# Optimization experiments

Hardware: AMD Instinct MI355X
Metric: run time of the kernel (lower is better)

The kernel has to match this reference:

```python
import jax, jax.numpy as jnp
import numpy as np

EMBED_DIM = 1024
NUM_HEADS = 16
HEAD_DIM = EMBED_DIM // NUM_HEADS
SCALING_FACTOR = 0.1
SCALING = (HEAD_DIM * SCALING_FACTOR) ** (-0.5)
B, L = 4, 1024


def setup_inputs() -> dict:
    key = jax.random.key(0)
    ks = jax.random.split(key, 8)
    query = jax.random.normal(ks[0], (B, L, EMBED_DIM), dtype=jnp.float32)
    key_padding_mask = jnp.zeros((B, L), dtype=bool)
    attn_bias = jax.random.normal(ks[1], (B * NUM_HEADS, L, L), dtype=jnp.float32)
    s_in = 1.0 / np.sqrt(EMBED_DIM)
    Wqkv = jax.random.normal(ks[2], (3 * EMBED_DIM, EMBED_DIM), dtype=jnp.float32) * s_in
    bqkv = jnp.zeros((3 * EMBED_DIM,), dtype=jnp.float32)
    Wo = jax.random.normal(ks[3], (EMBED_DIM, EMBED_DIM), dtype=jnp.float32) * s_in
    bo = jnp.zeros((EMBED_DIM,), dtype=jnp.float32)
    return {"query": query, "key_padding_mask": key_padding_mask, "attn_bias": attn_bias,
            "Wqkv": Wqkv, "bqkv": bqkv, "Wo": Wo, "bo": bo}


def reference(query, key_padding_mask, attn_bias, Wqkv, bqkv, Wo, bo):
    b, l, e = query.shape
    # fused in-projection: (B, L, 3E)
    qkv = jnp.einsum("ble,fe->blf", query, Wqkv) + bqkv
    q, k, v = jnp.split(qkv, 3, axis=-1)
    q = q * SCALING
    # (B, L, H, D)
    q = q.reshape(b, l, NUM_HEADS, HEAD_DIM)
    k = k.reshape(b, l, NUM_HEADS, HEAD_DIM)
    v = v.reshape(b, l, NUM_HEADS, HEAD_DIM)
    # scores: (B, H, L, L)
    scores = jnp.einsum("blhd,bmhd->bhlm", q, k)
    scores = scores + attn_bias.reshape(b, NUM_HEADS, l, l)
    neg_inf = jnp.asarray(-jnp.inf, scores.dtype)
    scores = jnp.where(key_padding_mask[:, None, None, :], neg_inf, scores)
    probs = jax.nn.softmax(scores, axis=-1)  # dropout: eval mode (identity)
    out = jnp.einsum("bhlm,bmhd->blhd", probs, v).reshape(b, l, e)
    return jnp.einsum("ble,fe->blf", out, Wo) + bo
```

## Files before the change

kernel.cpp:

```cpp
#include <hip/hip_runtime.h>
#include <math.h>

#define EMB   1024
#define NH    16
#define HD    64
#define BATCH 4
#define LSEQ  1024
#define NTOK  (BATCH*LSEQ)
#define SCALING 0.39528470752104744f

typedef __attribute__((ext_vector_type(8))) short short8;
typedef __attribute__((ext_vector_type(4))) float f32x4;

__device__ __forceinline__ float bf2f(short s) {
    union { float f; unsigned u; } x; x.u = ((unsigned)(unsigned short)s) << 16; return x.f;
}
__device__ __forceinline__ short f2bf(float f) {
    union { float f; unsigned u; } x; x.f = f;
    unsigned r = x.u + 0x7fff + ((x.u >> 16) & 1);
    return (short)(r >> 16);
}

__device__ __forceinline__ void glds16(const void* g, void* l) {
    __builtin_amdgcn_global_load_lds(
        (const __attribute__((address_space(1))) void*)g,
        (__attribute__((address_space(3))) void*)l, 16, 0, 0);
}

__global__ __launch_bounds__(256) void cvt_bf16(
    const float* __restrict__ in, short* __restrict__ out, int n)
{
    int i = (blockIdx.x * 256 + threadIdx.x) * 8;
    if (i >= n) return;
    float4 a = *(const float4*)(in + i);
    float4 b = *(const float4*)(in + i + 4);
    short8 o;
    o[0] = f2bf(a.x); o[1] = f2bf(a.y); o[2] = f2bf(a.z); o[3] = f2bf(a.w);
    o[4] = f2bf(b.x); o[5] = f2bf(b.y); o[6] = f2bf(b.z); o[7] = f2bf(b.w);
    *(short8*)(out + i) = o;
}

__global__ __launch_bounds__(256) void qkv_gemm(
    const short* __restrict__ X, const short* __restrict__ W,
    const float* __restrict__ bqkv,
    short* __restrict__ qws, short* __restrict__ kws, short* __restrict__ vws)
{
    __shared__ short As[128 * 32];
    __shared__ short Bs[128 * 32];
    const int tid = threadIdx.x;
    const int wave = tid >> 6, lane = tid & 63;
    const int quad = lane >> 4, l16 = lane & 15;
    const int m0 = blockIdx.y * 128, n0 = blockIdx.x * 128;
    const int wm = (wave >> 1) * 64, wn = (wave & 1) * 64;

    f32x4 acc[4][4] = {};

    const int srow = wave * 16 + (lane >> 2);
    const int scol = (lane & 3) * 16;

    const char* gA = (const char*)X + (size_t)(m0 + srow) * 2048 + scol;
    const char* gB = (const char*)W + (size_t)(n0 + srow) * 2048 + scol;
    char* lA = (char*)As + wave * 1024 + lane * 16;
    char* lB = (char*)Bs + wave * 1024 + lane * 16;

    for (int kt = 0; kt < 1024; kt += 32) {
        __syncthreads();
        const char* ga = gA + kt * 2;
        const char* gb = gB + kt * 2;
        glds16(ga, lA);
        glds16(ga + (size_t)64 * 2048, lA + 4096);
        glds16(gb, lB);
        glds16(gb + (size_t)64 * 2048, lB + 4096);
        __syncthreads();

        short8 af[4], bf[4];
        #pragma unroll
        for (int i = 0; i < 4; i++)
            af[i] = *(const short8*)((const char*)As + (wm + i * 16 + l16) * 64 + quad * 16);
        #pragma unroll
        for (int j = 0; j < 4; j++)
            bf[j] = *(const short8*)((const char*)Bs + (wn + j * 16 + l16) * 64 + quad * 16);
        #pragma unroll
        for (int i = 0; i < 4; i++)
            #pragma unroll
            for (int j = 0; j < 4; j++)
                acc[i][j] = __builtin_amdgcn_mfma_f32_16x16x32_bf16(af[i], bf[j], acc[i][j], 0, 0, 0);
    }

    #pragma unroll
    for (int i = 0; i < 4; i++) {
        #pragma unroll
        for (int j = 0; j < 4; j++) {
            #pragma unroll
            for (int r = 0; r < 4; r++) {
                int gm = m0 + wm + i * 16 + quad * 4 + r;
                int gn = n0 + wn + j * 16 + l16;
                float v = acc[i][j][r] + bqkv[gn];
                int part = gn >> 10;
                int cc = gn & 1023;
                int h = cc >> 6, d = cc & 63;
                int b = gm >> 10, l = gm & 1023;
                size_t dst = (((size_t)(b * NH + h)) * LSEQ + l) * HD + d;
                if (part == 0)      qws[dst] = f2bf(v * SCALING);
                else if (part == 1) kws[dst] = f2bf(v);
                else                vws[dst] = f2bf(v);
            }
        }
    }
}

__global__ __launch_bounds__(256) void attn_kernel(
    const short* __restrict__ qws, const short* __restrict__ kws,
    const short* __restrict__ vws, const float* __restrict__ bias,
    const unsigned char* __restrict__ mask, short* __restrict__ att)
{
    __shared__ short Qs[64 * 72];
    __shared__ short Ks[128 * 72];
    __shared__ short Vt[64 * 136];
    __shared__ short Ps[4 * 16 * 136];

    const int qt = blockIdx.x;
    const int bh = blockIdx.y;
    const int b = bh >> 4;
    const int tid = threadIdx.x, wave = tid >> 6, lane = tid & 63;
    const int quad = lane >> 4, l16 = lane & 15;
    const int h = bh & 15;

    const short* Qg = qws + (size_t)bh * LSEQ * HD + (size_t)qt * 64 * HD;
    const short* Kg = kws + (size_t)bh * LSEQ * HD;
    const short* Vg = vws + (size_t)bh * LSEQ * HD;
    const float* Bg = bias + (size_t)bh * LSEQ * LSEQ;

    #pragma unroll
    for (int i = 0; i < 2; i++) {
        int c = i * 256 + tid;
        int row = c >> 3, col8 = c & 7;
        *(int4*)((char*)Qs + row * 144 + col8 * 16) =
            *(const int4*)((const char*)Qg + row * 128 + col8 * 16);
    }

    float m_r[4], l_r[4];
    f32x4 o[4] = {};
    #pragma unroll
    for (int r = 0; r < 4; r++) { m_r[r] = -INFINITY; l_r[r] = 0.0f; }

    const int qrow_g = qt * 64 + wave * 16 + quad * 4;

    for (int kt0 = 0; kt0 < LSEQ; kt0 += 128) {
        __syncthreads();
        #pragma unroll
        for (int i = 0; i < 4; i++) {
            int c = i * 256 + tid;
            int row = c >> 3, col8 = c & 7;
            *(int4*)((char*)Ks + row * 144 + col8 * 16) =
                *(const int4*)((const char*)Kg + (size_t)(kt0 + row) * 128 + col8 * 16);
        }
        #pragma unroll
        for (int i = 0; i < 4; i++) {
            int c = i * 256 + tid;
            int row = c >> 3, col8 = c & 7;
            short8 v = *(const short8*)(Vg + (size_t)(kt0 + row) * HD + col8 * 8);
            #pragma unroll
            for (int j = 0; j < 8; j++)
                Vt[(col8 * 8 + j) * 136 + row] = v[j];
        }
        __syncthreads();

        short8 qf[2];
        #pragma unroll
        for (int ks = 0; ks < 2; ks++)
            qf[ks] = *(const short8*)((const char*)Qs + (wave * 16 + l16) * 144 + ks * 64 + quad * 16);
        f32x4 s[8] = {};
        #pragma unroll
        for (int ni = 0; ni < 8; ni++) {
            #pragma unroll
            for (int ks = 0; ks < 2; ks++) {
                short8 kf = *(const short8*)((const char*)Ks + (ni * 16 + l16) * 144 + ks * 64 + quad * 16);
                s[ni] = __builtin_amdgcn_mfma_f32_16x16x32_bf16(qf[ks], kf, s[ni], 0, 0, 0);
            }
        }

        #pragma unroll
        for (int ni = 0; ni < 8; ni++) {
            int col = kt0 + ni * 16 + l16;
            bool mk = mask[(size_t)b * LSEQ + col] != 0;
            #pragma unroll
            for (int r = 0; r < 4; r++) {
                float bv = Bg[(size_t)(qrow_g + r) * LSEQ + col];
                float val = s[ni][r] + bv;
                s[ni][r] = mk ? -INFINITY : val;
            }
        }

        #pragma unroll
        for (int r = 0; r < 4; r++) {
            float mx = s[0][r];
            #pragma unroll
            for (int ni = 1; ni < 8; ni++) mx = fmaxf(mx, s[ni][r]);
            #pragma unroll
            for (int off = 1; off < 16; off <<= 1)
                mx = fmaxf(mx, __shfl_xor(mx, off, 64));
            float mnew = fmaxf(m_r[r], mx);
            float alpha = (m_r[r] == -INFINITY) ? 0.0f : __expf(m_r[r] - mnew);
            m_r[r] = mnew;
            float sum = 0.0f;
            #pragma unroll
            for (int ni = 0; ni < 8; ni++) {
                float p = __expf(s[ni][r] - mnew);
                s[ni][r] = p;
                sum += p;
            }
            #pragma unroll
            for (int off = 1; off < 16; off <<= 1)
                sum += __shfl_xor(sum, off, 64);
            l_r[r] = l_r[r] * alpha + sum;
            #pragma unroll
            for (int ni2 = 0; ni2 < 4; ni2++) o[ni2][r] *= alpha;
            #pragma unroll
            for (int ni = 0; ni < 8; ni++)
                Ps[wave * 2176 + (quad * 4 + r) * 136 + ni * 16 + l16] = f2bf(s[ni][r]);
        }

        #pragma unroll
        for (int ks = 0; ks < 4; ks++) {
            short8 pf = *(const short8*)((const char*)Ps + wave * 4352 + l16 * 272 + ks * 64 + quad * 16);
            #pragma unroll
            for (int ni2 = 0; ni2 < 4; ni2++) {
                short8 vf = *(const short8*)((const char*)Vt + (ni2 * 16 + l16) * 272 + ks * 64 + quad * 16);
                o[ni2] = __builtin_amdgcn_mfma_f32_16x16x32_bf16(pf, vf, o[ni2], 0, 0, 0);
            }
        }
    }

    #pragma unroll
    for (int r = 0; r < 4; r++) {
        float inv = 1.0f / l_r[r];
        int lq = qt * 64 + wave * 16 + quad * 4 + r;
        #pragma unroll
        for (int ni2 = 0; ni2 < 4; ni2++) {
            int d = ni2 * 16 + l16;
            att[((size_t)(b * LSEQ + lq)) * EMB + h * HD + d] = f2bf(o[ni2][r] * inv);
        }
    }
}

__global__ __launch_bounds__(256) void out_gemm(
    const short* __restrict__ Xa, const short* __restrict__ Wo,
    const float* __restrict__ bo, float* __restrict__ out)
{
    __shared__ short As[128 * 32];
    __shared__ short Bs[128 * 32];
    const int tid = threadIdx.x;
    const int wave = tid >> 6, lane = tid & 63;
    const int quad = lane >> 4, l16 = lane & 15;
    const int m0 = blockIdx.y * 128, n0 = blockIdx.x * 128;
    const int wm = (wave >> 1) * 64, wn = (wave & 1) * 64;

    f32x4 acc[4][4] = {};

    const int srow = wave * 16 + (lane >> 2);
    const int scol = (lane & 3) * 16;
    const char* gA = (const char*)Xa + (size_t)(m0 + srow) * 2048 + scol;
    const char* gB = (const char*)Wo + (size_t)(n0 + srow) * 2048 + scol;
    char* lA = (char*)As + wave * 1024 + lane * 16;
    char* lB = (char*)Bs + wave * 1024 + lane * 16;

    for (int kt = 0; kt < 1024; kt += 32) {
        __syncthreads();
        const char* ga = gA + kt * 2;
        const char* gb = gB + kt * 2;
        glds16(ga, lA);
        glds16(ga + (size_t)64 * 2048, lA + 4096);
        glds16(gb, lB);
        glds16(gb + (size_t)64 * 2048, lB + 4096);
        __syncthreads();

        short8 af[4], bf[4];
        #pragma unroll
        for (int i = 0; i < 4; i++)
            af[i] = *(const short8*)((const char*)As + (wm + i * 16 + l16) * 64 + quad * 16);
        #pragma unroll
        for (int j = 0; j < 4; j++)
            bf[j] = *(const short8*)((const char*)Bs + (wn + j * 16 + l16) * 64 + quad * 16);
        #pragma unroll
        for (int i = 0; i < 4; i++)
            #pragma unroll
            for (int j = 0; j < 4; j++)
                acc[i][j] = __builtin_amdgcn_mfma_f32_16x16x32_bf16(af[i], bf[j], acc[i][j], 0, 0, 0);
    }

    #pragma unroll
    for (int i = 0; i < 4; i++) {
        #pragma unroll
        for (int j = 0; j < 4; j++) {
            #pragma unroll
            for (int r = 0; r < 4; r++) {
                int gm = m0 + wm + i * 16 + quad * 4 + r;
                int gn = n0 + wn + j * 16 + l16;
                out[(size_t)gm * EMB + gn] = acc[i][j][r] + bo[gn];
            }
        }
    }
}

extern "C" void kernel_launch(void* const* d_in, const int* in_sizes, int n_in,
                              void* d_out, int out_size, void* d_ws, size_t ws_size,
                              hipStream_t stream) {
    const float* query = (const float*)d_in[0];
    const unsigned char* mask = (const unsigned char*)d_in[1];
    const float* bias = (const float*)d_in[2];
    const float* Wqkv = (const float*)d_in[3];
    const float* bqkv = (const float*)d_in[4];
    const float* Wo   = (const float*)d_in[5];
    const float* bo   = (const float*)d_in[6];
    float* out = (float*)d_out;

    short* Xb  = (short*)d_ws;
    short* Wb  = Xb  + (size_t)4096 * 1024;
    short* Wob = Wb  + (size_t)3072 * 1024;
    short* qws = Wob + (size_t)1024 * 1024;
    short* kws = qws + (size_t)64 * 1024 * 64;
    short* vws = kws + (size_t)64 * 1024 * 64;
    short* att = vws + (size_t)64 * 1024 * 64;

    cvt_bf16<<<dim3(4096 * 1024 / 8 / 256), 256, 0, stream>>>(query, Xb, 4096 * 1024);
    cvt_bf16<<<dim3(3072 * 1024 / 8 / 256), 256, 0, stream>>>(Wqkv, Wb, 3072 * 1024);
    cvt_bf16<<<dim3(1024 * 1024 / 8 / 256), 256, 0, stream>>>(Wo, Wob, 1024 * 1024);

    qkv_gemm<<<dim3(24, 32), 256, 0, stream>>>(Xb, Wb, bqkv, qws, kws, vws);
    attn_kernel<<<dim3(16, 64), 256, 0, stream>>>(qws, kws, vws, bias, mask, att);
    out_gemm<<<dim3(8, 32), 256, 0, stream>>>(att, Wob, bo, out);
}
```

Before: 483.9 us.

## Fuse conversion kernels, prefetch bias and V in attention, swizzle LDS, retile out-GEMM

Merges the three fp32-to-bf16 conversion launches into a single kernel. In the attention kernel, Q fragments are loaded straight into registers, and the bias, mask and V tiles are prefetched into registers before the barrier. K is copied into LDS with direct global-to-LDS loads using an XOR swizzle, V is stored transposed with a swizzle to cut bank conflicts, and launch bounds request 3 blocks per CU. The output GEMM uses 128x64 tiles so twice as many blocks run. The changes aim to overlap the dominant bias reads with compute and improve occupancy, at the cost of more registers per thread.

```diff
diff --git a/kernel.cpp b/kernel.cpp
--- a/kernel.cpp
+++ b/kernel.cpp
@@ -27,17 +27,26 @@
         (__attribute__((address_space(3))) void*)l, 16, 0, 0);
 }
 
-__global__ __launch_bounds__(256) void cvt_bf16(
-    const float* __restrict__ in, short* __restrict__ out, int n)
+#define QCHUNKS  (4096*1024/8)
+#define WCHUNKS  (3072*1024/8)
+#define WOCHUNKS (1024*1024/8)
+__global__ __launch_bounds__(256) void cvt_all(
+    const float* __restrict__ q, const float* __restrict__ wqkv,
+    const float* __restrict__ wo,
+    short* __restrict__ xb, short* __restrict__ wb, short* __restrict__ wob)
 {
-    int i = (blockIdx.x * 256 + threadIdx.x) * 8;
-    if (i >= n) return;
-    float4 a = *(const float4*)(in + i);
-    float4 b = *(const float4*)(in + i + 4);
+    int c = blockIdx.x * 256 + threadIdx.x;
+    const float* src; short* dst; int off;
+    if (c < QCHUNKS)                { src = q;    dst = xb;  off = c; }
+    else if (c < QCHUNKS + WCHUNKS) { src = wqkv; dst = wb;  off = c - QCHUNKS; }
+    else                            { src = wo;   dst = wob; off = c - QCHUNKS - WCHUNKS; }
+    int i = off * 8;
+    float4 a = *(const float4*)(src + i);
+    float4 b = *(const float4*)(src + i + 4);
     short8 o;
     o[0] = f2bf(a.x); o[1] = f2bf(a.y); o[2] = f2bf(a.z); o[3] = f2bf(a.w);
     o[4] = f2bf(b.x); o[5] = f2bf(b.y); o[6] = f2bf(b.z); o[7] = f2bf(b.w);
-    *(short8*)(out + i) = o;
+    *(short8*)(dst + i) = o;
 }
 
 __global__ __launch_bounds__(256) void qkv_gemm(
@@ -109,13 +118,12 @@
     }
 }
 
-__global__ __launch_bounds__(256) void attn_kernel(
+__global__ __launch_bounds__(256, 3) void attn_kernel(
     const short* __restrict__ qws, const short* __restrict__ kws,
     const short* __restrict__ vws, const float* __restrict__ bias,
     const unsigned char* __restrict__ mask, short* __restrict__ att)
 {
-    __shared__ short Qs[64 * 72];
-    __shared__ short Ks[128 * 72];
+    __shared__ short Ks[128 * 64];
     __shared__ short Vt[64 * 136];
     __shared__ short Ps[4 * 16 * 136];
 
@@ -124,20 +132,16 @@
     const int b = bh >> 4;
     const int tid = threadIdx.x, wave = tid >> 6, lane = tid & 63;
     const int quad = lane >> 4, l16 = lane & 15;
-    const int h = bh & 15;
 
     const short* Qg = qws + (size_t)bh * LSEQ * HD + (size_t)qt * 64 * HD;
     const short* Kg = kws + (size_t)bh * LSEQ * HD;
     const short* Vg = vws + (size_t)bh * LSEQ * HD;
     const float* Bg = bias + (size_t)bh * LSEQ * LSEQ;
 
-    #pragma unroll
-    for (int i = 0; i < 2; i++) {
-        int c = i * 256 + tid;
-        int row = c >> 3, col8 = c & 7;
-        *(int4*)((char*)Qs + row * 144 + col8 * 16) =
-            *(const int4*)((const char*)Qg + row * 128 + col8 * 16);
-    }
+    short8 qf[2];
+    #pragma unroll
+    for (int ks = 0; ks < 2; ks++)
+        qf[ks] = *(const short8*)(Qg + (wave * 16 + l16) * HD + ks * 32 + quad * 8);
 
     float m_r[4], l_r[4];
     f32x4 o[4] = {};
@@ -145,50 +149,68 @@
     for (int r = 0; r < 4; r++) { m_r[r] = -INFINITY; l_r[r] = 0.0f; }
 
     const int qrow_g = qt * 64 + wave * 16 + quad * 4;
+    const float* Bp = Bg + (size_t)qrow_g * LSEQ + l16;
+    const unsigned char* Mp = mask + (size_t)b * LSEQ + l16;
 
     for (int kt0 = 0; kt0 < LSEQ; kt0 += 128) {
-        __syncthreads();
+        float bv[8][4];
+        #pragma unroll
+        for (int ni = 0; ni < 8; ni++)
+            #pragma unroll
+            for (int r = 0; r < 4; r++)
+                bv[ni][r] = Bp[(size_t)r * LSEQ + kt0 + ni * 16];
+        unsigned char mk[8];
+        #pragma unroll
+        for (int ni = 0; ni < 8; ni++) mk[ni] = Mp[kt0 + ni * 16];
+        short8 vst[4];
         #pragma unroll
         for (int i = 0; i < 4; i++) {
             int c = i * 256 + tid;
-            int row = c >> 3, col8 = c & 7;
-            *(int4*)((char*)Ks + row * 144 + col8 * 16) =
-                *(const int4*)((const char*)Kg + (size_t)(kt0 + row) * 128 + col8 * 16);
-        }
+            int row = c >> 3, c8 = c & 7;
+            vst[i] = *(const short8*)(Vg + (size_t)(kt0 + row) * HD + c8 * 8);
+        }
+
+        __syncthreads();
+
         #pragma unroll
         for (int i = 0; i < 4; i++) {
             int c = i * 256 + tid;
-            int row = c >> 3, col8 = c & 7;
-            short8 v = *(const short8*)(Vg + (size_t)(kt0 + row) * HD + col8 * 8);
-            #pragma unroll
-            for (int j = 0; j < 8; j++)
-                Vt[(col8 * 8 + j) * 136 + row] = v[j];
-        }
-        __syncthreads();
-
-        short8 qf[2];
-        #pragma unroll
-        for (int ks = 0; ks < 2; ks++)
-            qf[ks] = *(const short8*)((const char*)Qs + (wave * 16 + l16) * 144 + ks * 64 + quad * 16);
+            int row = c >> 3;
+            int u = (c & 7) ^ (row & 7);
+            glds16((const char*)Kg + (size_t)(kt0 + row) * 128 + u * 16,
+                   (char*)Ks + c * 16);
+        }
+        #pragma unroll
+        for (int i = 0; i < 4; i++) {
+            int c = i * 256 + tid;
+            int row = c >> 3, c8 = c & 7;
+            int rl = row & 7, ru = row >> 3;
+            #pragma unroll
+            for (int j = 0; j < 8; j++) {
+                int d = c8 * 8 + j;
+                Vt[d * 136 + ((ru ^ c8) & 15) * 8 + rl] = vst[i][j];
+            }
+        }
+        __syncthreads();
+
         f32x4 s[8] = {};
         #pragma unroll
         for (int ni = 0; ni < 8; ni++) {
+            int krow = ni * 16 + l16;
             #pragma unroll
             for (int ks = 0; ks < 2; ks++) {
-                short8 kf = *(const short8*)((const char*)Ks + (ni * 16 + l16) * 144 + ks * 64 + quad * 16);
+                int u = (ks * 4 + quad) ^ (krow & 7);
+                short8 kf = *(const short8*)((const char*)Ks + krow * 128 + u * 16);
                 s[ni] = __builtin_amdgcn_mfma_f32_16x16x32_bf16(qf[ks], kf, s[ni], 0, 0, 0);
             }
         }
 
         #pragma unroll
         for (int ni = 0; ni < 8; ni++) {
-            int col = kt0 + ni * 16 + l16;
-            bool mk = mask[(size_t)b * LSEQ + col] != 0;
             #pragma unroll
             for (int r = 0; r < 4; r++) {
-                float bv = Bg[(size_t)(qrow_g + r) * LSEQ + col];
-                float val = s[ni][r] + bv;
-                s[ni][r] = mk ? -INFINITY : val;
+                float val = s[ni][r] + bv[ni][r];
+                s[ni][r] = mk[ni] ? -INFINITY : val;
             }
         }
 
@@ -226,12 +248,15 @@
             short8 pf = *(const short8*)((const char*)Ps + wave * 4352 + l16 * 272 + ks * 64 + quad * 16);
             #pragma unroll
             for (int ni2 = 0; ni2 < 4; ni2++) {
-                short8 vf = *(const short8*)((const char*)Vt + (ni2 * 16 + l16) * 272 + ks * 64 + quad * 16);
+                int d = ni2 * 16 + l16;
+                int u = (ks * 4 + quad) ^ ((d >> 3) & 7);
+                short8 vf = *(const short8*)((const char*)Vt + d * 272 + u * 16);
                 o[ni2] = __builtin_amdgcn_mfma_f32_16x16x32_bf16(pf, vf, o[ni2], 0, 0, 0);
             }
         }
     }
 
+    const int h = bh & 15;
     #pragma unroll
     for (int r = 0; r < 4; r++) {
         float inv = 1.0f / l_r[r];
@@ -249,50 +274,48 @@
     const float* __restrict__ bo, float* __restrict__ out)
 {
     __shared__ short As[128 * 32];
-    __shared__ short Bs[128 * 32];
+    __shared__ short Bs[64 * 32];
     const int tid = threadIdx.x;
     const int wave = tid >> 6, lane = tid & 63;
     const int quad = lane >> 4, l16 = lane & 15;
-    const int m0 = blockIdx.y * 128, n0 = blockIdx.x * 128;
-    const int wm = (wave >> 1) * 64, wn = (wave & 1) * 64;
-
-    f32x4 acc[4][4] = {};
+    const int m0 = blockIdx.y * 128, n0 = blockIdx.x * 64;
+    const int wm = (wave >> 1) * 64, wn = (wave & 1) * 32;
+
+    f32x4 acc[4][2] = {};
 
     const int srow = wave * 16 + (lane >> 2);
     const int scol = (lane & 3) * 16;
     const char* gA = (const char*)Xa + (size_t)(m0 + srow) * 2048 + scol;
-    const char* gB = (const char*)Wo + (size_t)(n0 + srow) * 2048 + scol;
+    const char* gB = (const char*)Wo + (size_t)(n0 + (tid >> 2)) * 2048 + (tid & 3) * 16;
     char* lA = (char*)As + wave * 1024 + lane * 16;
-    char* lB = (char*)Bs + wave * 1024 + lane * 16;
+    char* lB = (char*)Bs + tid * 16;
 
     for (int kt = 0; kt < 1024; kt += 32) {
         __syncthreads();
         const char* ga = gA + kt * 2;
-        const char* gb = gB + kt * 2;
         glds16(ga, lA);
         glds16(ga + (size_t)64 * 2048, lA + 4096);
-        glds16(gb, lB);
-        glds16(gb + (size_t)64 * 2048, lB + 4096);
-        __syncthreads();
-
-        short8 af[4], bf[4];
+        glds16(gB + kt * 2, lB);
+        __syncthreads();
+
+        short8 af[4], bf[2];
         #pragma unroll
         for (int i = 0; i < 4; i++)
             af[i] = *(const short8*)((const char*)As + (wm + i * 16 + l16) * 64 + quad * 16);
         #pragma unroll
-        for (int j = 0; j < 4; j++)
+        for (int j = 0; j < 2; j++)
             bf[j] = *(const short8*)((const char*)Bs + (wn + j * 16 + l16) * 64 + quad * 16);
         #pragma unroll
         for (int i = 0; i < 4; i++)
             #pragma unroll
-            for (int j = 0; j < 4; j++)
+            for (int j = 0; j < 2; j++)
                 acc[i][j] = __builtin_amdgcn_mfma_f32_16x16x32_bf16(af[i], bf[j], acc[i][j], 0, 0, 0);
     }
 
     #pragma unroll
     for (int i = 0; i < 4; i++) {
         #pragma unroll
-        for (int j = 0; j < 4; j++) {
+        for (int j = 0; j < 2; j++) {
             #pragma unroll
             for (int r = 0; r < 4; r++) {
                 int gm = m0 + wm + i * 16 + quad * 4 + r;
@@ -323,11 +346,10 @@
     short* vws = kws + (size_t)64 * 1024 * 64;
     short* att = vws + (size_t)64 * 1024 * 64;
 
-    cvt_bf16<<<dim3(4096 * 1024 / 8 / 256), 256, 0, stream>>>(query, Xb, 4096 * 1024);
-    cvt_bf16<<<dim3(3072 * 1024 / 8 / 256), 256, 0, stream>>>(Wqkv, Wb, 3072 * 1024);
-    cvt_bf16<<<dim3(1024 * 1024 / 8 / 256), 256, 0, stream>>>(Wo, Wob, 1024 * 1024);
+    cvt_all<<<dim3((QCHUNKS + WCHUNKS + WOCHUNKS) / 256), 256, 0, stream>>>(
+        query, Wqkv, Wo, Xb, Wb, Wob);
 
     qkv_gemm<<<dim3(24, 32), 256, 0, stream>>>(Xb, Wb, bqkv, qws, kws, vws);
     attn_kernel<<<dim3(16, 64), 256, 0, stream>>>(qws, kws, vws, bias, mask, att);
-    out_gemm<<<dim3(8, 32), 256, 0, stream>>>(att, Wob, bo, out);
-}
+    out_gemm<<<dim3(16, 32), 256, 0, stream>>>(att, Wob, bo, out);
+}
```

Result: no change. 482.3 us (-0.3%).
